# Optimization experiments

Hardware: AMD Instinct MI355X
Metric: run time of the kernel (lower is better)

## Reference

```python
import jax, jax.numpy as jnp
import numpy as np

C = 16
CO = 16
H = 4
CH = CO // H
CPW = 2 * C


def setup_inputs() -> dict:
    key = jax.random.key(0)
    ks = jax.random.split(key, 12)
    B, N, Nk = 2, 1024, 1024
    s = 0.1
    return {
        "xq": jax.random.normal(ks[0], (B, N, C), jnp.float32),
        "xk": jax.random.normal(ks[1], (B, Nk, C), jnp.float32),
        # fc_w: Linear(2C,2C) -> ReLU -> Linear(2C,H) -> ReLU   (stored as [in,out])
        "w1": jax.random.normal(ks[2], (CPW, CPW), jnp.float32) * s,
        "b1": jax.random.normal(ks[3], (CPW,), jnp.float32) * s,
        "w2": jax.random.normal(ks[4], (CPW, H), jnp.float32) * s,
        "b2": jax.random.normal(ks[5], (H,), jnp.float32) * s,
        # fc_v: Linear(2C,Co) -> ReLU -> Linear(Co,Co) -> ReLU
        "v1": jax.random.normal(ks[6], (CPW, CO), jnp.float32) * s,
        "bv1": jax.random.normal(ks[7], (CO,), jnp.float32) * s,
        "v2": jax.random.normal(ks[8], (CO, CO), jnp.float32) * s,
        "bv2": jax.random.normal(ks[9], (CO,), jnp.float32) * s,
    }


def reference(xq, xk, w1, b1, w2, b2, v1, bv1, v2, bv2):
    B, N, _ = xq.shape
    Nk = xk.shape[1]
    # pad/add/subtract trick in the source reduces to concat(xq, xk - xq)
    diff = xk[:, None, :, :] - xq[:, :, None, :]               # [B,N,Nk,C]
    xq_b = jnp.broadcast_to(xq[:, :, None, :], diff.shape)     # [B,N,Nk,C]
    x_pw = jnp.concatenate([xq_b, diff], axis=-1)              # [B,N,Nk,2C]
    # fc_w -> logits [B,N,Nk,H], softmax over Nk
    hw = jax.nn.relu(x_pw @ w1 + b1)
    logits = jax.nn.relu(hw @ w2 + b2)
    weight = jax.nn.softmax(logits, axis=2)                    # [B,N,Nk,H]
    # fc_v -> value [B,N,Nk,H,Ch]
    hv = jax.nn.relu(x_pw @ v1 + bv1)
    value = jax.nn.relu(hv @ v2 + bv2).reshape(B, N, Nk, H, CH)
    out = jnp.einsum('bnkh,bnkhc->bnhc', weight, value)        # sum over Nk
    return out.reshape(B, N, CO)
```

## Files before the change

### kernel.cpp

```cpp
#include <hip/hip_runtime.h>
#include <hip/hip_bf16.h>
#include <math.h>

static constexpr int Cc   = 16;
static constexpr int COc  = 16;
static constexpr int Hh   = 4;
static constexpr int CPWc = 32;
static constexpr int NTH  = 256;
static constexpr int MTH  = 512;
static constexpr int TFH  = 768;

typedef _Float16 f16x2 __attribute__((ext_vector_type(2)));
typedef _Float16 f16x8 __attribute__((ext_vector_type(8)));
typedef __attribute__((ext_vector_type(4))) float f32x4v;

union F4 { float4 v; float f[4]; };
union H8 {
  f16x8 v8;
  struct { f16x2 q0, q1, q2, q3; } p;
  float4 f4;
};

__device__ __forceinline__ ushort f2h(float x) {
  _Float16 h = (_Float16)x;
  ushort u;
  __builtin_memcpy(&u, &h, 2);
  return u;
}
__device__ __forceinline__ f16x2 relu2(f16x2 x) {
  return __builtin_elementwise_max(x, (f16x2)(_Float16)0);
}

__global__ __launch_bounds__(NTH) void ppa_precompute(
    const float* __restrict__ xq, const float* __restrict__ xk,
    const float* __restrict__ w1, const float* __restrict__ b1,
    const float* __restrict__ v1, const float* __restrict__ bv1,
    const float* __restrict__ w2, const float* __restrict__ v2,
    float* __restrict__ aW, float* __restrict__ aV,
    ushort* __restrict__ cP,
    ushort* __restrict__ w2f, ushort* __restrict__ v2f,
    int BN, int BK, int Nk, int nRowBlocks) {
  const int t = threadIdx.x;

  if (blockIdx.x == nRowBlocks) {
    if (t < 64) {
      const int n = t & 15, g = t >> 4;
#pragma unroll
      for (int i = 0; i < 8; ++i) {
        const int k = g * 8 + i;
        w2f[t * 8 + i] = f2h(w2[k * Hh + (n >> 2)]);
        v2f[t * 8 + i] = f2h(0.5f * v2[(k & 15) * COc + n]);
      }
    }
    return;
  }

  __shared__ float sw1[CPWc * CPWc];
  __shared__ float sv1[CPWc * COc];
  __shared__ float sb1[CPWc];
  __shared__ float sbv1[COc];
  for (int i = t; i < CPWc * CPWc; i += NTH) sw1[i] = w1[i];
  for (int i = t; i < CPWc * COc; i += NTH) sv1[i] = v1[i];
  if (t < CPWc) sb1[t] = b1[t];
  if (t < COc) sbv1[t] = bv1[t];
  __syncthreads();

  const int r = blockIdx.x * 64 + (t >> 2);
  const int sub = t & 3;
  if (r >= BN + BK) return;
  const bool isQ = (r < BN);
  const int rr = isQ ? r : (r - BN);
  const float* src = isQ ? (xq + (size_t)rr * Cc) : (xk + (size_t)rr * Cc);

  float x[Cc];
#pragma unroll
  for (int i = 0; i < Cc; i += 4) {
    float4 v = *reinterpret_cast<const float4*>(src + i);
    x[i] = v.x; x[i + 1] = v.y; x[i + 2] = v.z; x[i + 3] = v.w;
  }

  if (isQ) {
    F4 o0, o1, ov;
#pragma unroll
    for (int jj = 0; jj < 8; ++jj) {
      const int j = sub * 8 + jj;
      float acc = sb1[j];
#pragma unroll
      for (int i = 0; i < Cc; ++i)
        acc += x[i] * (sw1[i * CPWc + j] - sw1[(i + Cc) * CPWc + j]);
      if (jj < 4) o0.f[jj] = acc; else o1.f[jj - 4] = acc;
    }
#pragma unroll
    for (int jj = 0; jj < 4; ++jj) {
      const int j = sub * 4 + jj;
      float acc = sbv1[j];
#pragma unroll
      for (int i = 0; i < Cc; ++i)
        acc += x[i] * (sv1[i * COc + j] - sv1[(i + Cc) * COc + j]);
      ov.f[jj] = acc;
    }
    float* ap = aW + (size_t)rr * CPWc + sub * 8;
    *reinterpret_cast<float4*>(ap) = o0.v;
    *reinterpret_cast<float4*>(ap + 4) = o1.v;
    *reinterpret_cast<float4*>(aV + (size_t)rr * COc + sub * 4) = ov.v;
  } else {
    float cw[8];
    float cv4[4];
#pragma unroll
    for (int jj = 0; jj < 8; ++jj) {
      const int j = sub * 8 + jj;
      float acc = 0.f;
#pragma unroll
      for (int i = 0; i < Cc; ++i) acc += x[i] * sw1[(i + Cc) * CPWc + j];
      cw[jj] = acc;
    }
#pragma unroll
    for (int jj = 0; jj < 4; ++jj) {
      const int j = sub * 4 + jj;
      float acc = 0.f;
#pragma unroll
      for (int i = 0; i < Cc; ++i) acc += x[i] * sv1[(i + Cc) * COc + j];
      cv4[jj] = acc;
    }
    const int bb = rr / Nk;
    const int kk = rr - bb * Nk;
    const int T = kk >> 4, mm = kk & 15;
    ushort* tp = cP + ((size_t)bb * (Nk >> 4) + T) * TFH;
    ushort4 h0, h1;
    h0.x = f2h(cw[0]); h0.y = f2h(cw[1]); h0.z = f2h(cw[2]); h0.w = f2h(cw[3]);
    h1.x = f2h(cw[4]); h1.y = f2h(cw[5]); h1.z = f2h(cw[6]); h1.w = f2h(cw[7]);
    ushort* wp = tp + (sub * 16 + mm) * 8;
    *reinterpret_cast<ushort4*>(wp) = h0;
    *reinterpret_cast<ushort4*>(wp + 4) = h1;
    ushort4 hv;
    hv.x = f2h(cv4[0]); hv.y = f2h(cv4[1]); hv.z = f2h(cv4[2]); hv.w = f2h(cv4[3]);
    const int gg = sub >> 1, half = sub & 1;
    *reinterpret_cast<ushort4*>(tp + 512 + (gg * 16 + mm) * 8 + half * 4) = hv;
  }
}

__global__ __launch_bounds__(MTH) void ppa_main_mfma(
    const float* __restrict__ aW, const float* __restrict__ aV,
    const ushort* __restrict__ cP,
    const ushort* __restrict__ w2f, const float* __restrict__ b2,
    const ushort* __restrict__ v2f, const float* __restrict__ bv2,
    float* __restrict__ out, int N, int Nk) {
  __shared__ float sro[8][COc];
  __shared__ float srl[8][Hh];

  const int t = threadIdx.x;
  const int lane = t & 63, w = t >> 6;
  const int q = w & 3;
  const int m = lane & 15;
  const int g = lane >> 4;
  const int gg = g & 1;
  const int l31 = lane & 31;
  const int hh = m >> 2;
  const int row0 = blockIdx.x * 2;
  const int row = row0 + (w >> 2);
  const int b = row0 / N;

  f16x2 a01, a23, a45, a67, av01, av23, av45, av67;
  {
    const float* aRow = aW + (size_t)row * CPWc + g * 8;
    F4 v0, v1;
    v0.v = *reinterpret_cast<const float4*>(aRow);
    v1.v = *reinterpret_cast<const float4*>(aRow + 4);
    a01 = f16x2{(_Float16)v0.f[0], (_Float16)v0.f[1]};
    a23 = f16x2{(_Float16)v0.f[2], (_Float16)v0.f[3]};
    a45 = f16x2{(_Float16)v1.f[0], (_Float16)v1.f[1]};
    a67 = f16x2{(_Float16)v1.f[2], (_Float16)v1.f[3]};
    const float* avRow = aV + (size_t)row * COc + gg * 8;
    F4 u0, u1;
    u0.v = *reinterpret_cast<const float4*>(avRow);
    u1.v = *reinterpret_cast<const float4*>(avRow + 4);
    av01 = f16x2{(_Float16)u0.f[0], (_Float16)u0.f[1]};
    av23 = f16x2{(_Float16)u0.f[2], (_Float16)u0.f[3]};
    av45 = f16x2{(_Float16)u1.f[0], (_Float16)u1.f[1]};
    av67 = f16x2{(_Float16)u1.f[2], (_Float16)u1.f[3]};
  }
  const f16x8 wfrag = *reinterpret_cast<const f16x8*>(w2f + lane * 8);
  const f16x8 vfrag = *reinterpret_cast<const f16x8*>(v2f + lane * 8);
  const float b2h = b2[hh];
  const float bv2c = bv2[m];
  const f32x4v cbW = {b2h, b2h, b2h, b2h};
  const f32x4v cbV = {bv2c, bv2c, bv2c, bv2c};

  float o_acc = 0.f, l_acc = 0.f;

  const ushort* tb = cP + ((size_t)b * (Nk >> 4) + (size_t)q * 16) * TFH;

  H8 cw, cv;
  cw.f4 = *reinterpret_cast<const float4*>(tb + lane * 8);
  cv.f4 = *reinterpret_cast<const float4*>(tb + 512 + l31 * 8);

#pragma unroll
  for (int s = 0; s < 16; ++s) {
    H8 nw, nv;
    nw.f4 = float4{0.f, 0.f, 0.f, 0.f};
    nv.f4 = float4{0.f, 0.f, 0.f, 0.f};
    if (s < 15) {
      const ushort* nb = tb + (size_t)(s + 1) * TFH;
      nw.f4 = *reinterpret_cast<const float4*>(nb + lane * 8);
      nv.f4 = *reinterpret_cast<const float4*>(nb + 512 + l31 * 8);
    }

    H8 fw;
    fw.p.q0 = relu2(a01 + cw.p.q0);
    fw.p.q1 = relu2(a23 + cw.p.q1);
    fw.p.q2 = relu2(a45 + cw.p.q2);
    fw.p.q3 = relu2(a67 + cw.p.q3);
    const f32x4v lgD =
        __builtin_amdgcn_mfma_f32_16x16x32_f16(fw.v8, wfrag, cbW, 0, 0, 0);

    const float p0 = __expf(fmaxf(lgD[0], 0.f));
    const float p1 = __expf(fmaxf(lgD[1], 0.f));
    const float p2 = __expf(fmaxf(lgD[2], 0.f));
    const float p3 = __expf(fmaxf(lgD[3], 0.f));
    if ((m & 3) == 0) l_acc += (p0 + p1) + (p2 + p3);

    H8 fv;
    fv.p.q0 = relu2(av01 + cv.p.q0);
    fv.p.q1 = relu2(av23 + cv.p.q1);
    fv.p.q2 = relu2(av45 + cv.p.q2);
    fv.p.q3 = relu2(av67 + cv.p.q3);
    const f32x4v vD =
        __builtin_amdgcn_mfma_f32_16x16x32_f16(fv.v8, vfrag, cbV, 0, 0, 0);

    o_acc += p0 * fmaxf(vD[0], 0.f);
    o_acc += p1 * fmaxf(vD[1], 0.f);
    o_acc += p2 * fmaxf(vD[2], 0.f);
    o_acc += p3 * fmaxf(vD[3], 0.f);

    cw = nw; cv = nv;
  }

  o_acc += __shfl_xor(o_acc, 16);
  o_acc += __shfl_xor(o_acc, 32);
  l_acc += __shfl_xor(l_acc, 16);
  l_acc += __shfl_xor(l_acc, 32);
  if (lane < COc) sro[w][m] = o_acc;
  if (lane < COc && (lane & 3) == 0) srl[w][lane >> 2] = l_acc;
  __syncthreads();

  if (t < 2 * COc) {
    const int r = t >> 4, c = t & 15, h = c >> 2;
    const int wb = r * 4;
    const float osum = (sro[wb][c] + sro[wb + 1][c]) +
                       (sro[wb + 2][c] + sro[wb + 3][c]);
    const float lsum = (srl[wb][h] + srl[wb + 1][h]) +
                       (srl[wb + 2][h] + srl[wb + 3][h]);
    out[(size_t)(row0 + r) * COc + c] = osum / lsum;
  }
}

extern "C" void kernel_launch(void* const* d_in, const int* in_sizes, int n_in,
                              void* d_out, int out_size, void* d_ws, size_t ws_size,
                              hipStream_t stream) {
  const float* xq  = (const float*)d_in[0];
  const float* xk  = (const float*)d_in[1];
  const float* w1  = (const float*)d_in[2];
  const float* b1  = (const float*)d_in[3];
  const float* w2  = (const float*)d_in[4];
  const float* b2  = (const float*)d_in[5];
  const float* v1  = (const float*)d_in[6];
  const float* bv1 = (const float*)d_in[7];
  const float* v2  = (const float*)d_in[8];
  const float* bv2 = (const float*)d_in[9];
  float* out = (float*)d_out;

  const int BN = in_sizes[0] / Cc;
  const int BK = in_sizes[1] / Cc;
  const int B = 2;
  const int N = BN / B;
  const int Nk = BK / B;

  float* ws = (float*)d_ws;
  float* aW = ws;
  float* aV = aW + (size_t)BN * CPWc;
  ushort* cP = (ushort*)(aV + (size_t)BN * COc);
  ushort* w2f = cP + (size_t)BK * 48;
  ushort* v2f = w2f + 64 * 8;

  const int totalRows = BN + BK;
  const int nRowBlocks = (totalRows + 63) / 64;
  ppa_precompute<<<nRowBlocks + 1, NTH, 0, stream>>>(
      xq, xk, w1, b1, v1, bv1, w2, v2,
      aW, aV, cP, w2f, v2f, BN, BK, Nk, nRowBlocks);
  ppa_main_mfma<<<BN / 2, MTH, 0, stream>>>(aW, aV, cP, w2f, b2, v2f, bv2,
                                            out, N, Nk);
}
```

Baseline: 25.72 us.

## Share key tiles across both query rows in each wave to halve tile loads

Each wave now processes both query rows of the block against half of its key range, rather than one row against the full range. Each loaded key tile (cw/cv) is therefore reused for two rows, which halves global/L2 tile traffic per MFMA and doubles the independent MFMA chains per iteration for better ILP. The cost is more registers for the duplicated row activations and accumulators, and an 8-way shared-memory reduction at the end instead of a 4-way one.

```diff
diff --git a/kernel.cpp b/kernel.cpp
--- a/kernel.cpp
+++ b/kernel.cpp
@@ -145,39 +145,54 @@
     const ushort* __restrict__ w2f, const float* __restrict__ b2,
     const ushort* __restrict__ v2f, const float* __restrict__ bv2,
     float* __restrict__ out, int N, int Nk) {
-  __shared__ float sro[8][COc];
-  __shared__ float srl[8][Hh];
+  __shared__ float sro[8][2][COc];
+  __shared__ float srl[8][2][Hh];
 
   const int t = threadIdx.x;
   const int lane = t & 63, w = t >> 6;
   const int q = w & 3;
+  const int half = w >> 2;
   const int m = lane & 15;
   const int g = lane >> 4;
   const int gg = g & 1;
   const int l31 = lane & 31;
   const int hh = m >> 2;
   const int row0 = blockIdx.x * 2;
-  const int row = row0 + (w >> 2);
   const int b = row0 / N;
 
-  f16x2 a01, a23, a45, a67, av01, av23, av45, av67;
+  f16x2 a0_0, a0_1, a0_2, a0_3, av0_0, av0_1, av0_2, av0_3;
+  f16x2 a1_0, a1_1, a1_2, a1_3, av1_0, av1_1, av1_2, av1_3;
   {
-    const float* aRow = aW + (size_t)row * CPWc + g * 8;
-    F4 v0, v1;
-    v0.v = *reinterpret_cast<const float4*>(aRow);
-    v1.v = *reinterpret_cast<const float4*>(aRow + 4);
-    a01 = f16x2{(_Float16)v0.f[0], (_Float16)v0.f[1]};
-    a23 = f16x2{(_Float16)v0.f[2], (_Float16)v0.f[3]};
-    a45 = f16x2{(_Float16)v1.f[0], (_Float16)v1.f[1]};
-    a67 = f16x2{(_Float16)v1.f[2], (_Float16)v1.f[3]};
-    const float* avRow = aV + (size_t)row * COc + gg * 8;
-    F4 u0, u1;
-    u0.v = *reinterpret_cast<const float4*>(avRow);
-    u1.v = *reinterpret_cast<const float4*>(avRow + 4);
-    av01 = f16x2{(_Float16)u0.f[0], (_Float16)u0.f[1]};
-    av23 = f16x2{(_Float16)u0.f[2], (_Float16)u0.f[3]};
-    av45 = f16x2{(_Float16)u1.f[0], (_Float16)u1.f[1]};
-    av67 = f16x2{(_Float16)u1.f[2], (_Float16)u1.f[3]};
+    const float* aR0 = aW + (size_t)row0 * CPWc + g * 8;
+    const float* aR1 = aW + (size_t)(row0 + 1) * CPWc + g * 8;
+    F4 v0, v1, u0, u1;
+    v0.v = *reinterpret_cast<const float4*>(aR0);
+    v1.v = *reinterpret_cast<const float4*>(aR0 + 4);
+    u0.v = *reinterpret_cast<const float4*>(aR1);
+    u1.v = *reinterpret_cast<const float4*>(aR1 + 4);
+    a0_0 = f16x2{(_Float16)v0.f[0], (_Float16)v0.f[1]};
+    a0_1 = f16x2{(_Float16)v0.f[2], (_Float16)v0.f[3]};
+    a0_2 = f16x2{(_Float16)v1.f[0], (_Float16)v1.f[1]};
+    a0_3 = f16x2{(_Float16)v1.f[2], (_Float16)v1.f[3]};
+    a1_0 = f16x2{(_Float16)u0.f[0], (_Float16)u0.f[1]};
+    a1_1 = f16x2{(_Float16)u0.f[2], (_Float16)u0.f[3]};
+    a1_2 = f16x2{(_Float16)u1.f[0], (_Float16)u1.f[1]};
+    a1_3 = f16x2{(_Float16)u1.f[2], (_Float16)u1.f[3]};
+    const float* vR0 = aV + (size_t)row0 * COc + gg * 8;
+    const float* vR1 = aV + (size_t)(row0 + 1) * COc + gg * 8;
+    F4 w0, w1v, x0, x1;
+    w0.v = *reinterpret_cast<const float4*>(vR0);
+    w1v.v = *reinterpret_cast<const float4*>(vR0 + 4);
+    x0.v = *reinterpret_cast<const float4*>(vR1);
+    x1.v = *reinterpret_cast<const float4*>(vR1 + 4);
+    av0_0 = f16x2{(_Float16)w0.f[0], (_Float16)w0.f[1]};
+    av0_1 = f16x2{(_Float16)w0.f[2], (_Float16)w0.f[3]};
+    av0_2 = f16x2{(_Float16)w1v.f[0], (_Float16)w1v.f[1]};
+    av0_3 = f16x2{(_Float16)w1v.f[2], (_Float16)w1v.f[3]};
+    av1_0 = f16x2{(_Float16)x0.f[0], (_Float16)x0.f[1]};
+    av1_1 = f16x2{(_Float16)x0.f[2], (_Float16)x0.f[3]};
+    av1_2 = f16x2{(_Float16)x1.f[0], (_Float16)x1.f[1]};
+    av1_3 = f16x2{(_Float16)x1.f[2], (_Float16)x1.f[3]};
   }
   const f16x8 wfrag = *reinterpret_cast<const f16x8*>(w2f + lane * 8);
   const f16x8 vfrag = *reinterpret_cast<const f16x8*>(v2f + lane * 8);
@@ -186,70 +201,102 @@
   const f32x4v cbW = {b2h, b2h, b2h, b2h};
   const f32x4v cbV = {bv2c, bv2c, bv2c, bv2c};
 
-  float o_acc = 0.f, l_acc = 0.f;
-
-  const ushort* tb = cP + ((size_t)b * (Nk >> 4) + (size_t)q * 16) * TFH;
+  float o0 = 0.f, l0 = 0.f, o1 = 0.f, l1 = 0.f;
+
+  const ushort* tb =
+      cP + ((size_t)b * (Nk >> 4) + (size_t)q * 16 + (size_t)half * 8) * TFH;
 
   H8 cw, cv;
   cw.f4 = *reinterpret_cast<const float4*>(tb + lane * 8);
   cv.f4 = *reinterpret_cast<const float4*>(tb + 512 + l31 * 8);
 
 #pragma unroll
-  for (int s = 0; s < 16; ++s) {
+  for (int s = 0; s < 8; ++s) {
     H8 nw, nv;
     nw.f4 = float4{0.f, 0.f, 0.f, 0.f};
     nv.f4 = float4{0.f, 0.f, 0.f, 0.f};
-    if (s < 15) {
+    if (s < 7) {
       const ushort* nb = tb + (size_t)(s + 1) * TFH;
       nw.f4 = *reinterpret_cast<const float4*>(nb + lane * 8);
       nv.f4 = *reinterpret_cast<const float4*>(nb + 512 + l31 * 8);
     }
 
-    H8 fw;
-    fw.p.q0 = relu2(a01 + cw.p.q0);
-    fw.p.q1 = relu2(a23 + cw.p.q1);
-    fw.p.q2 = relu2(a45 + cw.p.q2);
-    fw.p.q3 = relu2(a67 + cw.p.q3);
-    const f32x4v lgD =
-        __builtin_amdgcn_mfma_f32_16x16x32_f16(fw.v8, wfrag, cbW, 0, 0, 0);
-
-    const float p0 = __expf(fmaxf(lgD[0], 0.f));
-    const float p1 = __expf(fmaxf(lgD[1], 0.f));
-    const float p2 = __expf(fmaxf(lgD[2], 0.f));
-    const float p3 = __expf(fmaxf(lgD[3], 0.f));
-    if ((m & 3) == 0) l_acc += (p0 + p1) + (p2 + p3);
-
-    H8 fv;
-    fv.p.q0 = relu2(av01 + cv.p.q0);
-    fv.p.q1 = relu2(av23 + cv.p.q1);
-    fv.p.q2 = relu2(av45 + cv.p.q2);
-    fv.p.q3 = relu2(av67 + cv.p.q3);
-    const f32x4v vD =
-        __builtin_amdgcn_mfma_f32_16x16x32_f16(fv.v8, vfrag, cbV, 0, 0, 0);
-
-    o_acc += p0 * fmaxf(vD[0], 0.f);
-    o_acc += p1 * fmaxf(vD[1], 0.f);
-    o_acc += p2 * fmaxf(vD[2], 0.f);
-    o_acc += p3 * fmaxf(vD[3], 0.f);
+    H8 fw0, fw1;
+    fw0.p.q0 = relu2(a0_0 + cw.p.q0);
+    fw0.p.q1 = relu2(a0_1 + cw.p.q1);
+    fw0.p.q2 = relu2(a0_2 + cw.p.q2);
+    fw0.p.q3 = relu2(a0_3 + cw.p.q3);
+    const f32x4v lg0 =
+        __builtin_amdgcn_mfma_f32_16x16x32_f16(fw0.v8, wfrag, cbW, 0, 0, 0);
+    fw1.p.q0 = relu2(a1_0 + cw.p.q0);
+    fw1.p.q1 = relu2(a1_1 + cw.p.q1);
+    fw1.p.q2 = relu2(a1_2 + cw.p.q2);
+    fw1.p.q3 = relu2(a1_3 + cw.p.q3);
+    const f32x4v lg1 =
+        __builtin_amdgcn_mfma_f32_16x16x32_f16(fw1.v8, wfrag, cbW, 0, 0, 0);
+
+    const float p00 = __expf(fmaxf(lg0[0], 0.f));
+    const float p01 = __expf(fmaxf(lg0[1], 0.f));
+    const float p02 = __expf(fmaxf(lg0[2], 0.f));
+    const float p03 = __expf(fmaxf(lg0[3], 0.f));
+    const float p10 = __expf(fmaxf(lg1[0], 0.f));
+    const float p11 = __expf(fmaxf(lg1[1], 0.f));
+    const float p12 = __expf(fmaxf(lg1[2], 0.f));
+    const float p13 = __expf(fmaxf(lg1[3], 0.f));
+    if ((m & 3) == 0) {
+      l0 += (p00 + p01) + (p02 + p03);
+      l1 += (p10 + p11) + (p12 + p13);
+    }
+
+    H8 fv0, fv1;
+    fv0.p.q0 = relu2(av0_0 + cv.p.q0);
+    fv0.p.q1 = relu2(av0_1 + cv.p.q1);
+    fv0.p.q2 = relu2(av0_2 + cv.p.q2);
+    fv0.p.q3 = relu2(av0_3 + cv.p.q3);
+    const f32x4v vD0 =
+        __builtin_amdgcn_mfma_f32_16x16x32_f16(fv0.v8, vfrag, cbV, 0, 0, 0);
+    fv1.p.q0 = relu2(av1_0 + cv.p.q0);
+    fv1.p.q1 = relu2(av1_1 + cv.p.q1);
+    fv1.p.q2 = relu2(av1_2 + cv.p.q2);
+    fv1.p.q3 = relu2(av1_3 + cv.p.q3);
+    const f32x4v vD1 =
+        __builtin_amdgcn_mfma_f32_16x16x32_f16(fv1.v8, vfrag, cbV, 0, 0, 0);
+
+    o0 += p00 * fmaxf(vD0[0], 0.f);
+    o0 += p01 * fmaxf(vD0[1], 0.f);
+    o0 += p02 * fmaxf(vD0[2], 0.f);
+    o0 += p03 * fmaxf(vD0[3], 0.f);
+    o1 += p10 * fmaxf(vD1[0], 0.f);
+    o1 += p11 * fmaxf(vD1[1], 0.f);
+    o1 += p12 * fmaxf(vD1[2], 0.f);
+    o1 += p13 * fmaxf(vD1[3], 0.f);
 
     cw = nw; cv = nv;
   }
 
-  o_acc += __shfl_xor(o_acc, 16);
-  o_acc += __shfl_xor(o_acc, 32);
-  l_acc += __shfl_xor(l_acc, 16);
-  l_acc += __shfl_xor(l_acc, 32);
-  if (lane < COc) sro[w][m] = o_acc;
-  if (lane < COc && (lane & 3) == 0) srl[w][lane >> 2] = l_acc;
+  o0 += __shfl_xor(o0, 16);
+  o0 += __shfl_xor(o0, 32);
+  o1 += __shfl_xor(o1, 16);
+  o1 += __shfl_xor(o1, 32);
+  l0 += __shfl_xor(l0, 16);
+  l0 += __shfl_xor(l0, 32);
+  l1 += __shfl_xor(l1, 16);
+  l1 += __shfl_xor(l1, 32);
+  if (lane < COc) { sro[w][0][m] = o0; sro[w][1][m] = o1; }
+  if (lane < COc && (lane & 3) == 0) {
+    srl[w][0][lane >> 2] = l0;
+    srl[w][1][lane >> 2] = l1;
+  }
   __syncthreads();
 
   if (t < 2 * COc) {
     const int r = t >> 4, c = t & 15, h = c >> 2;
-    const int wb = r * 4;
-    const float osum = (sro[wb][c] + sro[wb + 1][c]) +
-                       (sro[wb + 2][c] + sro[wb + 3][c]);
-    const float lsum = (srl[wb][h] + srl[wb + 1][h]) +
-                       (srl[wb + 2][h] + srl[wb + 3][h]);
+    float osum = 0.f, lsum = 0.f;
+#pragma unroll
+    for (int ww = 0; ww < 8; ++ww) {
+      osum += sro[ww][r][c];
+      lsum += srl[ww][r][h];
+    }
     out[(size_t)(row0 + r) * COc + c] = osum / lsum;
   }
 }
```

Result: no change. 25.44 us (-1.1%).
